# Kernel optimization log

Measured on AMD Instinct MI355X. Metric: run time of the kernel, lower is better.

The kernel has to match this reference:

```python
import jax, jax.numpy as jnp
import numpy as np

SIZE = 201
SIGMA = 25.0
PAD = SIZE // 2  # 100


def _gauss_kernel():
    # matches gauss(201, 25): unnormalized Gaussian pdf samples on [-100, 100]
    r = np.arange(-PAD, PAD + 1, dtype=np.float32)
    k = np.exp(-(r ** 2) / (2.0 * SIGMA ** 2)) / (SIGMA * np.sqrt(2.0 * np.pi))
    return jnp.asarray(k, dtype=jnp.float32)


def setup_inputs() -> dict:
    key = jax.random.key(0)
    x = jax.random.uniform(key, (64, 544, 960), dtype=jnp.float32)  # [T, H, W]
    return {"x": x}


def reference(x):
    # Separable Gaussian blur: 201-tap kernel along H, then along W, 'same' padding.
    # Faithful to the torch code, where the pad-then-crop on the other dims is a no-op.
    k = _gauss_kernel()
    T, H, W = x.shape
    xi = x[:, None, :, :]                       # [T, 1, H, W] -> batch over frames
    kh = k.reshape(1, 1, SIZE, 1)               # OIHW kernel along H
    kw = k.reshape(1, 1, 1, SIZE)               # OIHW kernel along W
    dn = jax.lax.conv_dimension_numbers(xi.shape, kh.shape, ('NCHW', 'OIHW', 'NCHW'))
    y = jax.lax.conv_general_dilated(xi, kh, (1, 1), [(PAD, PAD), (0, 0)], dimension_numbers=dn)
    y = jax.lax.conv_general_dilated(y, kw, (1, 1), [(0, 0), (PAD, PAD)], dimension_numbers=dn)
    return y.reshape(1, 1, T, H, W)             # original returns [1, 1, T, H, W]
```

## Files before the change

kernel.cpp:

```cpp
#include <hip/hip_runtime.h>


typedef _Float16 half8 __attribute__((ext_vector_type(8)));
typedef float    f32x4 __attribute__((ext_vector_type(4)));
typedef unsigned short u16;
typedef unsigned int   u32;

#define HH   544
#define WWD  960
#define PADC 100
#define RV   32

constexpr double cexp_taylor(double x) {
  double term = 1.0, sum = 1.0;
  for (int n = 1; n < 120; ++n) { term *= x / n; sum += term; }
  return sum;
}
constexpr float gaussk(int k) {
  if (k < 0 || k > 200) return 0.0f;
  double r = (double)(k - PADC);
  return (float)(cexp_taylor(-(r * r) / (2.0 * 25.0 * 25.0))
                 / (25.0 * 2.5066282746310002));
}

struct G0T { float v[288]; };
constexpr G0T make_g0() {
  G0T t{};
  for (int i = 0; i < 288; ++i) t.v[i] = gaussk(i - 40);
  return t;
}
__device__ __constant__ G0T G0 = make_g0();

__device__ __forceinline__ u16 f16u(float x) {
  return __builtin_bit_cast(u16, (_Float16)x);
}

template<int R, int C, bool IN16>
__global__ __launch_bounds__(256, 3) void gconv2(const void* __restrict__ inv,
                                                 void* __restrict__ outv) {
  constexpr int MB  = (R + 127) / 128;
  constexpr int NB  = (C + 127) / 128;
  constexpr int BPF = MB * NB;

  const int lid = blockIdx.x;
  const int xcd = lid & 7;
  const int s   = lid >> 3;
  const int f   = s / BPF;
  const int rb_ = s - f * BPF;
  const int tf  = (f << 3) | xcd;
  const int mb  = rb_ / NB;
  const int nb  = rb_ - mb * NB;
  const int m0  = mb * 128, n0 = nb * 128;
  const int imax = ((R - m0) >> 4) < 8 ? ((R - m0) >> 4) : 8;
  const int Tblk = ((16 * imax + 215) >> 5) + 1;

  const int tid = threadIdx.x;
  const size_t fofs = (size_t)tf * R * C;

  __shared__ uint4 PF[15][64];
  __shared__ uint4 Bbuf[2][512];

  for (int E = tid; E < 960; E += 256) {
    const int le = E & 63, uq = E >> 6;
    const int bas = (le & 15) - 8 * (le >> 4) + 16 * uq + 32;
    u32 w[4];
#pragma unroll
    for (int p = 0; p < 4; ++p) {
      const u16 h0 = f16u(G0.v[bas - 2 * p] * 1024.0f);
      const u16 h1 = f16u(G0.v[bas - 2 * p - 1] * 1024.0f);
      w[p] = (u32)h0 | ((u32)h1 << 16);
    }
    uint4 q; q.x = w[0]; q.y = w[1]; q.z = w[2]; q.w = w[3];
    PF[uq][le] = q;
  }

  const int nl   = tid & 63;
  const int wv   = tid >> 6;
  const int n16  = nl & 15, g4 = nl >> 4;
  const int cc0  = n0 + 2 * nl;
  const int ccl  = cc0 < C - 2 ? cc0 : C - 2;
  const int kb0  = m0 - PADC;
  const int swW  = wv ^ (nl & 3);
  const int ggB  = g4 ^ ((n16 >> 1) & 3);
  const int colA = 32 * wv + n16;

  const float* inF = (const float*)inv + fofs + ccl;
  const u16*   inH = (const u16*)inv + fofs + ccl;

  float2 ldf[8];
  u32    ldh[8];

  auto LOADREGS = [&](int t) {
    const int rbase = kb0 + 32 * t + 8 * wv;
#pragma unroll
    for (int j = 0; j < 8; ++j) {
      const int rr = rbase + j;
      const bool ok = (rr >= 0) && (rr < R);
      if constexpr (!IN16) {
        ldf[j] = ok ? *(const float2*)(inF + (size_t)rr * C)
                    : make_float2(0.f, 0.f);
      } else {
        ldh[j] = ok ? *(const u32*)(inH + (size_t)rr * C) : 0u;
      }
    }
  };

  f32x4 acc[8][2];
#pragma unroll
  for (int i = 0; i < 8; ++i) {
    acc[i][0] = (f32x4){0.f, 0.f, 0.f, 0.f};
    acc[i][1] = (f32x4){0.f, 0.f, 0.f, 0.f};
  }

  LOADREGS(0);

  for (int t = 0; t < Tblk; ++t) {
    uint4 qx, qy;
    if constexpr (!IN16) {
      u32 px[4], py[4];
#pragma unroll
      for (int p = 0; p < 4; ++p) {
        const float2 v0 = ldf[2 * p], v1 = ldf[2 * p + 1];
        px[p] = (u32)f16u(v0.x) | ((u32)f16u(v1.x) << 16);
        py[p] = (u32)f16u(v0.y) | ((u32)f16u(v1.y) << 16);
      }
      qx.x = px[0]; qx.y = px[1]; qx.z = px[2]; qx.w = px[3];
      qy.x = py[0]; qy.y = py[1]; qy.z = py[2]; qy.w = py[3];
    } else {
      qx.x = (ldh[0] & 0xffffu) | (ldh[1] << 16);
      qx.y = (ldh[2] & 0xffffu) | (ldh[3] << 16);
      qx.z = (ldh[4] & 0xffffu) | (ldh[5] << 16);
      qx.w = (ldh[6] & 0xffffu) | (ldh[7] << 16);
      qy.x = (ldh[0] >> 16) | (ldh[1] & 0xffff0000u);
      qy.y = (ldh[2] >> 16) | (ldh[3] & 0xffff0000u);
      qy.z = (ldh[4] >> 16) | (ldh[5] & 0xffff0000u);
      qy.w = (ldh[6] >> 16) | (ldh[7] & 0xffff0000u);
    }

    if (t + 1 < Tblk) LOADREGS(t + 1);

    Bbuf[t & 1][(2 * nl) * 4 + swW]     = qx;
    Bbuf[t & 1][(2 * nl + 1) * 4 + swW] = qy;
    __syncthreads();

    const half8 b0 = *reinterpret_cast<const half8*>(&Bbuf[t & 1][colA * 4 + ggB]);
    const half8 b1 = *reinterpret_cast<const half8*>(&Bbuf[t & 1][(colA + 16) * 4 + ggB]);
#pragma unroll
    for (int i = 0; i < 8; ++i) {
      const int tlo = i >> 1;
      if (i < imax && t >= tlo && t <= tlo + 6 + (i & 1)) {
        const half8 a = *reinterpret_cast<const half8*>(&PF[i - 2 * t + 13][nl]);
        acc[i][0] = __builtin_amdgcn_mfma_f32_16x16x32_f16(a, b0, acc[i][0], 0, 0, 0);
        acc[i][1] = __builtin_amdgcn_mfma_f32_16x16x32_f16(a, b1, acc[i][1], 0, 0, 0);
      }
    }
  }

  const float SDE = 1.0f / 1024.0f;
#pragma unroll
  for (int nt = 0; nt < 2; ++nt) {
    const int c_out = n0 + colA + 16 * nt;
    if (((C & 127) == 0) || (c_out < C)) {
      if constexpr (!IN16) {
        u16* of = (u16*)outv + fofs + (size_t)c_out * R;
#pragma unroll
        for (int i = 0; i < 8; ++i) {
          if (i < imax) {
            const int r0 = m0 + 16 * i + 4 * g4;
            uint2 o;
            o.x = (u32)f16u(acc[i][nt][0] * SDE) | ((u32)f16u(acc[i][nt][1] * SDE) << 16);
            o.y = (u32)f16u(acc[i][nt][2] * SDE) | ((u32)f16u(acc[i][nt][3] * SDE) << 16);
            *(uint2*)(of + r0) = o;
          }
        }
      } else {
        float* of = (float*)outv + fofs + (size_t)c_out * R;
#pragma unroll
        for (int i = 0; i < 8; ++i) {
          if (i < imax) {
            const int r0 = m0 + 16 * i + 4 * g4;
            float4 o;
            o.x = acc[i][nt][0] * SDE; o.y = acc[i][nt][1] * SDE;
            o.z = acc[i][nt][2] * SDE; o.w = acc[i][nt][3] * SDE;
            *(float4*)(of + r0) = o;
          }
        }
      }
    }
  }
}

struct KTabZ { float v[272]; };
constexpr KTabZ make_ktz() {
  KTabZ t{};
  for (int i = 0; i < 272; ++i) t.v[i] = gaussk(i - 31);
  return t;
}
__device__ __constant__ KTabZ KTZ = make_ktz();

struct KTabE { float v[216]; };
constexpr KTabE make_kte() {
  KTabE t{};
  for (int i = 0; i < 216; ++i) t.v[i] = gaussk(i - 8);
  return t;
}
__device__ __constant__ KTabE KTE = make_kte();

__global__ __launch_bounds__(256, 4) void vpass(const float* __restrict__ x,
                                                float* __restrict__ y) {
  const int lid = blockIdx.x;
  const int xcd = lid & 7;
  const int s   = lid >> 3;
  const int f   = s / 34;
  const int r34 = s - 34 * f;
  const int t   = (f << 3) | xcd;
  const int wt  = r34 & 1;
  const int hc  = r34 >> 1;
  const int tid = threadIdx.x;
  const int w   = 2 * (wt * 256 + tid);
  const int h0  = hc * RV;
  if (w >= WWD) return;

  const float* xw = x + (size_t)t * (HH * WWD) + w;

  float ax[RV], ay[RV];
#pragma unroll
  for (int r = 0; r < RV; ++r) { ax[r] = 0.f; ay[r] = 0.f; }

#pragma unroll 8
  for (int bb = 0; bb < 232; ++bb) {
    const int h  = h0 + bb - PADC;
    const int hcl = (h < 0) ? 0 : ((h > HH - 1) ? HH - 1 : h);
    const float m = (h == hcl) ? 1.0f : 0.0f;
    float2 v = *(const float2*)(xw + (size_t)hcl * WWD);
    v.x *= m; v.y *= m;
    const float* kb = &KTZ.v[bb + 31];
#pragma unroll
    for (int r = 0; r < RV; ++r) {
      const float kk = kb[-r];
      ax[r] = fmaf(kk, v.x, ax[r]);
      ay[r] = fmaf(kk, v.y, ay[r]);
    }
  }

  float* yp = y + (size_t)t * (HH * WWD) + (size_t)h0 * WWD + w;
#pragma unroll
  for (int r = 0; r < RV; ++r) {
    float2 o; o.x = ax[r]; o.y = ay[r];
    *(float2*)(yp + (size_t)r * WWD) = o;
  }
}

__device__ __forceinline__ int swz(int q) { return q ^ ((q >> 3) & 1); }

__global__ __launch_bounds__(256, 4) void hpass(float* __restrict__ y) {
  __shared__ __align__(16) float4 row[2][292];
  const int tid = threadIdx.x;
  const int hh  = tid >> 7;
  const int lt  = tid & 127;
  float* yp = y + (size_t)(blockIdx.x * 2 + hh) * WWD;

  const float4 z4 = {0.f, 0.f, 0.f, 0.f};
  if (lt < 25) {
    row[hh][swz(lt)] = z4;
  } else if (lt >= 32 && lt < 57) {
    row[hh][swz(265 + lt - 32)] = z4;
  }
  if (lt < 120) {
    const int q0 = 25 + 2 * lt;
    row[hh][swz(q0)]     = *(const float4*)(yp + 8 * lt);
    row[hh][swz(q0 + 1)] = *(const float4*)(yp + 8 * lt + 4);
  }
  __syncthreads();

  if (lt < 120) {
    float a0=0.f,a1=0.f,a2=0.f,a3=0.f,a4=0.f,a5=0.f,a6=0.f,a7=0.f;
#pragma unroll 4
    for (int j = 0; j < 52; ++j) {
      const float4 v = row[hh][swz(2 * lt + j)];
      const float* kb = &KTE.v[4 * j + 8];
      {
        const float xv = v.x;
        a0 = fmaf(kb[0], xv, a0);  a1 = fmaf(kb[-1], xv, a1);
        a2 = fmaf(kb[-2], xv, a2); a3 = fmaf(kb[-3], xv, a3);
        a4 = fmaf(kb[-4], xv, a4); a5 = fmaf(kb[-5], xv, a5);
        a6 = fmaf(kb[-6], xv, a6); a7 = fmaf(kb[-7], xv, a7);
      }
      {
        const float xv = v.y;
        a0 = fmaf(kb[1], xv, a0);  a1 = fmaf(kb[0], xv, a1);
        a2 = fmaf(kb[-1], xv, a2); a3 = fmaf(kb[-2], xv, a3);
        a4 = fmaf(kb[-3], xv, a4); a5 = fmaf(kb[-4], xv, a5);
        a6 = fmaf(kb[-5], xv, a6); a7 = fmaf(kb[-6], xv, a7);
      }
      {
        const float xv = v.z;
        a0 = fmaf(kb[2], xv, a0);  a1 = fmaf(kb[1], xv, a1);
        a2 = fmaf(kb[0], xv, a2);  a3 = fmaf(kb[-1], xv, a3);
        a4 = fmaf(kb[-2], xv, a4); a5 = fmaf(kb[-3], xv, a5);
        a6 = fmaf(kb[-4], xv, a6); a7 = fmaf(kb[-5], xv, a7);
      }
      {
        const float xv = v.w;
        a0 = fmaf(kb[3], xv, a0);  a1 = fmaf(kb[2], xv, a1);
        a2 = fmaf(kb[1], xv, a2);  a3 = fmaf(kb[0], xv, a3);
        a4 = fmaf(kb[-1], xv, a4); a5 = fmaf(kb[-2], xv, a5);
        a6 = fmaf(kb[-3], xv, a6); a7 = fmaf(kb[-4], xv, a7);
      }
    }
    float4 o0; o0.x = a0; o0.y = a1; o0.z = a2; o0.w = a3;
    float4 o1; o1.x = a4; o1.y = a5; o1.z = a6; o1.w = a7;
    *(float4*)(yp + 8 * lt)     = o0;
    *(float4*)(yp + 8 * lt + 4) = o1;
  }
}

extern "C" void kernel_launch(void* const* d_in, const int* in_sizes, int n_in,
                              void* d_out, int out_size, void* d_ws, size_t ws_size,
                              hipStream_t stream) {
  const float* x = (const float*)d_in[0];
  float* out = (float*)d_out;
  (void)in_sizes; (void)n_in; (void)out_size;

  const size_t ws_need = (size_t)64 * HH * WWD * sizeof(u16);
  if (d_ws != nullptr && ws_size >= ws_need) {
    u16* mid = (u16*)d_ws;
    gconv2<HH, WWD, false><<<dim3(2560), dim3(256), 0, stream>>>((const void*)x, (void*)mid);
    gconv2<WWD, HH, true ><<<dim3(2560), dim3(256), 0, stream>>>((const void*)mid, (void*)out);
  } else {
    vpass<<<dim3(2 * (HH / RV) * 64), dim3(256), 0, stream>>>(x, out);
    hpass<<<dim3(64 * HH / 2), dim3(256), 0, stream>>>(out);
  }
}
```

Before: 361.9 us.

## Double-buffer global loads, skip zero-padded row tiles, raise occupancy and MFMA priority

The banded MFMA convolution kernel now prefetches two K-steps ahead using ping-pong register sets, and it limits the K loop to tiles that hold in-range rows, so steps that would only read zero padding are skipped. The __syncthreads is replaced by an explicit LDS waitcnt plus s_barrier with a sched_barrier, and the MFMA block runs at raised wave priority. Launch bounds go from 3 to 4 waves per SIMD. The extra prefetch registers compete with the higher occupancy target and may cause spills.

Measured after the change: 352.4 us. 1.03x faster.

```diff
diff --git a/kernel.cpp b/kernel.cpp
--- a/kernel.cpp
+++ b/kernel.cpp
@@ -36,7 +36,7 @@
 }
 
 template<int R, int C, bool IN16>
-__global__ __launch_bounds__(256, 3) void gconv2(const void* __restrict__ inv,
+__global__ __launch_bounds__(256, 4) void gconv3(const void* __restrict__ inv,
                                                  void* __restrict__ outv) {
   constexpr int MB  = (R + 127) / 128;
   constexpr int NB  = (C + 127) / 128;
@@ -54,6 +54,10 @@
   const int imax = ((R - m0) >> 4) < 8 ? ((R - m0) >> 4) : 8;
   const int Tblk = ((16 * imax + 215) >> 5) + 1;
 
+  const int t_lo = (m0 >= 69) ? 0 : ((100 - m0) >> 5);
+  int t_hi = (R + 99 - m0) / 32 + 1;
+  if (t_hi > Tblk) t_hi = Tblk;
+
   const int tid = threadIdx.x;
   const size_t fofs = (size_t)tf * R * C;
 
@@ -87,22 +91,23 @@
   const float* inF = (const float*)inv + fofs + ccl;
   const u16*   inH = (const u16*)inv + fofs + ccl;
 
-  float2 ldf[8];
-  u32    ldh[8];
-
-  auto LOADREGS = [&](int t) {
+  float2 lfA[8], lfB[8];
+  u32    lhA[8], lhB[8];
+
+  auto loadregs = [&](int t, float2 (&lf)[8], u32 (&lh)[8]) {
     const int rbase = kb0 + 32 * t + 8 * wv;
 #pragma unroll
     for (int j = 0; j < 8; ++j) {
       const int rr = rbase + j;
       const bool ok = (rr >= 0) && (rr < R);
       if constexpr (!IN16) {
-        ldf[j] = ok ? *(const float2*)(inF + (size_t)rr * C)
-                    : make_float2(0.f, 0.f);
+        lf[j] = ok ? *(const float2*)(inF + (size_t)rr * C)
+                   : make_float2(0.f, 0.f);
       } else {
-        ldh[j] = ok ? *(const u32*)(inH + (size_t)rr * C) : 0u;
-      }
-    }
+        lh[j] = ok ? *(const u32*)(inH + (size_t)rr * C) : 0u;
+      }
+    }
+    (void)lf; (void)lh;
   };
 
   f32x4 acc[8][2];
@@ -112,39 +117,41 @@
     acc[i][1] = (f32x4){0.f, 0.f, 0.f, 0.f};
   }
 
-  LOADREGS(0);
-
-  for (int t = 0; t < Tblk; ++t) {
+  auto step = [&](int t, float2 (&lf)[8], u32 (&lh)[8]) {
     uint4 qx, qy;
     if constexpr (!IN16) {
       u32 px[4], py[4];
 #pragma unroll
       for (int p = 0; p < 4; ++p) {
-        const float2 v0 = ldf[2 * p], v1 = ldf[2 * p + 1];
+        const float2 v0 = lf[2 * p], v1 = lf[2 * p + 1];
         px[p] = (u32)f16u(v0.x) | ((u32)f16u(v1.x) << 16);
         py[p] = (u32)f16u(v0.y) | ((u32)f16u(v1.y) << 16);
       }
       qx.x = px[0]; qx.y = px[1]; qx.z = px[2]; qx.w = px[3];
       qy.x = py[0]; qy.y = py[1]; qy.z = py[2]; qy.w = py[3];
     } else {
-      qx.x = (ldh[0] & 0xffffu) | (ldh[1] << 16);
-      qx.y = (ldh[2] & 0xffffu) | (ldh[3] << 16);
-      qx.z = (ldh[4] & 0xffffu) | (ldh[5] << 16);
-      qx.w = (ldh[6] & 0xffffu) | (ldh[7] << 16);
-      qy.x = (ldh[0] >> 16) | (ldh[1] & 0xffff0000u);
-      qy.y = (ldh[2] >> 16) | (ldh[3] & 0xffff0000u);
-      qy.z = (ldh[4] >> 16) | (ldh[5] & 0xffff0000u);
-      qy.w = (ldh[6] >> 16) | (ldh[7] & 0xffff0000u);
-    }
-
-    if (t + 1 < Tblk) LOADREGS(t + 1);
+      qx.x = (lh[0] & 0xffffu) | (lh[1] << 16);
+      qx.y = (lh[2] & 0xffffu) | (lh[3] << 16);
+      qx.z = (lh[4] & 0xffffu) | (lh[5] << 16);
+      qx.w = (lh[6] & 0xffffu) | (lh[7] << 16);
+      qy.x = (lh[0] >> 16) | (lh[1] & 0xffff0000u);
+      qy.y = (lh[2] >> 16) | (lh[3] & 0xffff0000u);
+      qy.z = (lh[4] >> 16) | (lh[5] & 0xffff0000u);
+      qy.w = (lh[6] >> 16) | (lh[7] & 0xffff0000u);
+    }
+
+    if (t + 2 < t_hi) loadregs(t + 2, lf, lh);
 
     Bbuf[t & 1][(2 * nl) * 4 + swW]     = qx;
     Bbuf[t & 1][(2 * nl + 1) * 4 + swW] = qy;
-    __syncthreads();
+
+    asm volatile("s_waitcnt lgkmcnt(0)" ::: "memory");
+    __builtin_amdgcn_s_barrier();
+    __builtin_amdgcn_sched_barrier(0);
 
     const half8 b0 = *reinterpret_cast<const half8*>(&Bbuf[t & 1][colA * 4 + ggB]);
     const half8 b1 = *reinterpret_cast<const half8*>(&Bbuf[t & 1][(colA + 16) * 4 + ggB]);
+    __builtin_amdgcn_s_setprio(1);
 #pragma unroll
     for (int i = 0; i < 8; ++i) {
       const int tlo = i >> 1;
@@ -154,6 +161,15 @@
         acc[i][1] = __builtin_amdgcn_mfma_f32_16x16x32_f16(a, b1, acc[i][1], 0, 0, 0);
       }
     }
+    __builtin_amdgcn_s_setprio(0);
+  };
+
+  loadregs(t_lo, lfA, lhA);
+  if (t_lo + 1 < t_hi) loadregs(t_lo + 1, lfB, lhB);
+
+  for (int t = t_lo; t < t_hi; t += 2) {
+    step(t, lfA, lhA);
+    if (t + 1 < t_hi) step(t + 1, lfB, lhB);
   }
 
   const float SDE = 1.0f / 1024.0f;
@@ -325,8 +341,8 @@
   const size_t ws_need = (size_t)64 * HH * WWD * sizeof(u16);
   if (d_ws != nullptr && ws_size >= ws_need) {
     u16* mid = (u16*)d_ws;
-    gconv2<HH, WWD, false><<<dim3(2560), dim3(256), 0, stream>>>((const void*)x, (void*)mid);
-    gconv2<WWD, HH, true ><<<dim3(2560), dim3(256), 0, stream>>>((const void*)mid, (void*)out);
+    gconv3<HH, WWD, false><<<dim3(2560), dim3(256), 0, stream>>>((const void*)x, (void*)mid);
+    gconv3<WWD, HH, true ><<<dim3(2560), dim3(256), 0, stream>>>((const void*)mid, (void*)out);
   } else {
     vpass<<<dim3(2 * (HH / RV) * 64), dim3(256), 0, stream>>>(x, out);
     hpass<<<dim3(64 * HH / 2), dim3(256), 0, stream>>>(out);
```
